# Kernel tuning notes

Measured on AMD Instinct MI355X. Metric: run time of the kernel, lower is better.

The kernel has to match this reference:

```python
import jax, jax.numpy as jnp
import numpy as np
import math

DIM = 2048
N_HEADS = 32
N_KV_HEADS = 8
HEAD_DIM = DIM // N_HEADS  # 64
N_REP = N_HEADS // N_KV_HEADS  # 4
BATCH = 1
SEQ = 2048


def rope_cos_sin(seq_len, head_dim, dtype=jnp.float32):
    inv_freq = 1.0 / (10000.0 ** (jnp.arange(0, head_dim, 2, dtype=jnp.float32) / head_dim))
    t = jnp.arange(seq_len, dtype=jnp.float32)
    freqs = jnp.outer(t, inv_freq)            # [S, D/2]
    emb = jnp.concatenate([freqs, freqs], -1)  # [S, D]
    return jnp.cos(emb).astype(dtype), jnp.sin(emb).astype(dtype)


def rotate_half(x):
    x1 = x[..., ::2]
    x2 = x[..., 1::2]
    return jnp.concatenate([-x2, x1], axis=-1)


def setup_inputs() -> dict:
    key = jax.random.key(0)
    ks = jax.random.split(key, 5)
    scale = 1.0 / math.sqrt(DIM)
    x = jax.random.normal(ks[0], (BATCH, SEQ, DIM), jnp.float32)
    wq = jax.random.normal(ks[1], (DIM, N_HEADS * HEAD_DIM), jnp.float32) * scale
    wk = jax.random.normal(ks[2], (DIM, N_KV_HEADS * HEAD_DIM), jnp.float32) * scale
    wv = jax.random.normal(ks[3], (DIM, N_KV_HEADS * HEAD_DIM), jnp.float32) * scale
    wo = jax.random.normal(ks[4], (N_HEADS * HEAD_DIM, DIM), jnp.float32) * scale
    mask = jnp.tril(jnp.ones((SEQ, SEQ), jnp.int32))[None, None]  # [1,1,S,S]
    return {"x": x, "mask": mask, "wq": wq, "wk": wk, "wv": wv, "wo": wo}


def reference(x, mask, wq, wk, wv, wo):
    B, S, _ = x.shape
    q = (x @ wq).reshape(B, S, N_HEADS, HEAD_DIM).transpose(0, 2, 1, 3)     # [B,H,S,D]
    k = (x @ wk).reshape(B, S, N_KV_HEADS, HEAD_DIM).transpose(0, 2, 1, 3)  # [B,Hkv,S,D]
    v = (x @ wv).reshape(B, S, N_KV_HEADS, HEAD_DIM).transpose(0, 2, 1, 3)
    cos, sin = rope_cos_sin(S, HEAD_DIM)  # [S,D]
    q = q * cos + rotate_half(q) * sin
    k = k * cos + rotate_half(k) * sin
    if N_REP > 1:
        k = jnp.repeat(k, N_REP, axis=1)
        v = jnp.repeat(v, N_REP, axis=1)
    scores = jnp.einsum("bhqd,bhkd->bhqk", q, k) / math.sqrt(HEAD_DIM)
    scores = jnp.where(mask == 0, -jnp.inf, scores)
    attn = jax.nn.softmax(scores, axis=-1)
    out = jnp.einsum("bhqk,bhkd->bhqd", attn, v)  # [B,H,S,D]
    out = out.transpose(0, 2, 1, 3).reshape(B, S, N_HEADS * HEAD_DIM)
    return out @ wo
```

## Files before the change

### kernel.cpp

```cpp
#include <hip/hip_runtime.h>
#include <hip/hip_bf16.h>

#define DIM 2048
#define SEQ 2048
#define NH 32
#define HD 64
#define NKV 8
#define QKV_LD 3072

typedef __attribute__((ext_vector_type(8))) short bf16x8;
typedef __attribute__((ext_vector_type(4))) float f32x4;
typedef __attribute__((ext_vector_type(2))) unsigned int uint2v;
typedef unsigned short ushort_t;

__device__ inline unsigned short f2bf(float f) {
    union { float f; unsigned int u; } v; v.f = f;
    unsigned int r = v.u + 0x7fffu + ((v.u >> 16) & 1u);
    return (unsigned short)(r >> 16);
}
__device__ inline float bf2f(ushort_t u) {
    union { unsigned int u; float f; } v; v.u = ((unsigned int)u) << 16; return v.f;
}

__device__ inline void async_cp16(const void* g, void* l) {
    __builtin_amdgcn_global_load_lds(
        (const __attribute__((address_space(1))) unsigned int*)g,
        (__attribute__((address_space(3))) unsigned int*)l, 16, 0, 0);
}

__device__ inline void pswap32(unsigned int& a, unsigned int& b) {
    uint2v r = __builtin_amdgcn_permlane32_swap(a, b, false, false);
    a = r[0]; b = r[1];
}
__device__ inline void pswap16(unsigned int& a, unsigned int& b) {
    uint2v r = __builtin_amdgcn_permlane16_swap(a, b, false, false);
    a = r[0]; b = r[1];
}
__device__ inline float wave_max(float x) {
    unsigned int a = __float_as_uint(x), b = a;
    uint2v r = __builtin_amdgcn_permlane16_swap(a, b, false, false);
    x = fmaxf(__uint_as_float(r[0]), __uint_as_float(r[1]));
    a = __float_as_uint(x); b = a;
    r = __builtin_amdgcn_permlane32_swap(a, b, false, false);
    return fmaxf(__uint_as_float(r[0]), __uint_as_float(r[1]));
}
__device__ inline float wave_sum(float x) {
    unsigned int a = __float_as_uint(x), b = a;
    uint2v r = __builtin_amdgcn_permlane16_swap(a, b, false, false);
    x = __uint_as_float(r[0]) + __uint_as_float(r[1]);
    a = __float_as_uint(x); b = a;
    r = __builtin_amdgcn_permlane32_swap(a, b, false, false);
    return __uint_as_float(r[0]) + __uint_as_float(r[1]);
}
__device__ inline unsigned int cvt_pk_bf16(float lo, float hi) {
    unsigned int r;
    asm volatile("v_cvt_pk_bf16_f32 %0, %1, %2" : "=v"(r) : "v"(lo), "v"(hi));
    return r;
}

__global__ __launch_bounds__(256) void convert_kernel(
    const float* __restrict__ X, ushort_t* __restrict__ Xb)
{
    int i = (blockIdx.x * 256 + threadIdx.x) * 4;
    float4 v = *(const float4*)(X + i);
    ushort_t o[4] = { f2bf(v.x), f2bf(v.y), f2bf(v.z), f2bf(v.w) };
    *(uint2*)(Xb + i) = *(uint2*)o;
}

__global__ __launch_bounds__(256) void transpose_kernel(
    const float* __restrict__ W, ushort_t* __restrict__ WT, int N)
{
    __shared__ __align__(16) ushort_t tile[64][72];
    const int n0 = blockIdx.x * 64, k0 = blockIdx.y * 64;
    const int t = threadIdx.x;
    {
        const int tk = t >> 4;
        const int tn = (t & 15) * 4;
        #pragma unroll
        for (int i = 0; i < 4; i++) {
            const int k = tk + i * 16;
            float4 v = *(const float4*)(W + (size_t)(k0 + k) * N + n0 + tn);
            tile[tn + 0][k] = f2bf(v.x);
            tile[tn + 1][k] = f2bf(v.y);
            tile[tn + 2][k] = f2bf(v.z);
            tile[tn + 3][k] = f2bf(v.w);
        }
    }
    __syncthreads();
    {
        const int tn = t >> 2;
        const int tk = (t & 3) * 16;
        uint4 a = *(const uint4*)&tile[tn][tk];
        uint4 b = *(const uint4*)&tile[tn][tk + 8];
        ushort_t* dst = WT + (size_t)(n0 + tn) * DIM + k0 + tk;
        *(uint4*)dst = a;
        *(uint4*)(dst + 8) = b;
    }
}

template<int OUT_F32>
__global__ __launch_bounds__(256) void gemm_kernel(
    const ushort_t* __restrict__ A, const ushort_t* __restrict__ BT,
    void* __restrict__ Cout, int K, int lda, int ldo)
{
    __shared__ __align__(16) ushort_t sA[128 * 32];
    __shared__ __align__(16) ushort_t sB[64 * 32];
    const int tn = blockIdx.x * 64, tm = blockIdx.y * 128;
    const int t = threadIdx.x, wave = t >> 6, lane = t & 63;
    const int m16 = lane & 15, quad = lane >> 4;
    const int wr = (wave >> 1) * 64, wc = (wave & 1) * 32;
    const int srow = lane >> 2;
    const int sce = (lane & 3) * 8;

    f32x4 acc[4][2] = {};

    for (int k0 = 0; k0 < K; k0 += 32) {
        __syncthreads();
        #pragma unroll
        for (int p = 0; p < 2; p++) {
            const int j = wave * 2 + p;
            const int row = j * 16 + srow;
            async_cp16(A + (size_t)(tm + row) * lda + k0 + sce, &sA[j * 512]);
        }
        async_cp16(BT + (size_t)(tn + wave * 16 + srow) * K + k0 + sce, &sB[wave * 512]);
        __syncthreads();
        bf16x8 af[4], bf[2];
        #pragma unroll
        for (int mt = 0; mt < 4; mt++)
            af[mt] = *(const bf16x8*)&sA[(wr + mt * 16 + m16) * 32 + quad * 8];
        #pragma unroll
        for (int nt = 0; nt < 2; nt++)
            bf[nt] = *(const bf16x8*)&sB[(wc + nt * 16 + m16) * 32 + quad * 8];
        #pragma unroll
        for (int mt = 0; mt < 4; mt++)
            #pragma unroll
            for (int nt = 0; nt < 2; nt++)
                acc[mt][nt] = __builtin_amdgcn_mfma_f32_16x16x32_bf16(af[mt], bf[nt], acc[mt][nt], 0, 0, 0);
    }

    #pragma unroll
    for (int mt = 0; mt < 4; mt++) {
        const int row = tm + wr + mt * 16 + quad * 4;
        #pragma unroll
        for (int nt = 0; nt < 2; nt++) {
            const int col = tn + wc + nt * 16 + m16;
            #pragma unroll
            for (int r = 0; r < 4; r++) {
                if (OUT_F32)
                    ((float*)Cout)[(size_t)(row + r) * ldo + col] = acc[mt][nt][r];
                else
                    ((ushort_t*)Cout)[(size_t)(row + r) * ldo + col] = f2bf(acc[mt][nt][r]);
            }
        }
    }
}

#define QSCALE 0.18033688011112042f
__global__ __launch_bounds__(256) void rope_kernel(ushort_t* qkv, ushort_t* __restrict__ Kr)
{
    const int gid = blockIdx.x * 256 + threadIdx.x;
    const int lane = gid & 63;
    const int idx = gid >> 6;
    const int s = idx / 40;
    const int hh = idx - s * 40;

    const ushort_t* src;
    ushort_t* dst;
    const bool isq = (hh < 32);
    if (isq) {
        dst = qkv + (size_t)s * QKV_LD + hh * 64;
        src = dst;
    } else {
        src = qkv + (size_t)s * QKV_LD + 2048 + (hh - 32) * 64;
        dst = Kr + ((size_t)(hh - 32) * SEQ + s) * 64;
    }

    const float e = bf2f(src[lane]);
    const int i = lane & 31;
    const float freq = __expf(-(float)i * 0.28782313662425572f);
    const float ang = (float)s * freq;
    const float cv = cosf(ang), sv = sinf(ang);
    const int partner = (lane < 32) ? (2 * lane + 1) : (2 * (lane - 32));
    const float y = __shfl(e, partner, 64);
    float out = (lane < 32) ? (e * cv - y * sv) : (e * cv + y * sv);
    if (isq) out *= QSCALE;
    dst[lane] = f2bf(out);
}

__global__ __launch_bounds__(256) void vtrans_kernel(
    const ushort_t* __restrict__ qkv, ushort_t* __restrict__ Vt)
{
    __shared__ __align__(16) ushort_t tile[64][72];
    const int kvh = blockIdx.x & 7;
    const int s0 = (blockIdx.x >> 3) * 64;
    const int t = threadIdx.x;
    {
        const int sr = t >> 3;
        const int d8 = (t & 7) * 8;
        #pragma unroll
        for (int i = 0; i < 2; i++) {
            const int s = sr + i * 32;
            ushort_t tmp[8];
            *(uint4*)tmp = *(const uint4*)(qkv + (size_t)(s0 + s) * QKV_LD + 2560 + kvh * 64 + d8);
            #pragma unroll
            for (int j = 0; j < 8; j++) tile[d8 + j][s] = tmp[j];
        }
    }
    __syncthreads();
    {
        const int dr = t >> 3;
        const int s8 = (t & 7) * 8;
        #pragma unroll
        for (int i = 0; i < 2; i++) {
            const int d = dr + i * 32;
            *(uint4*)(Vt + ((size_t)kvh * 64 + d) * SEQ + s0 + s8) = *(const uint4*)&tile[d][s8];
        }
    }
}

#define MFMA16(A, B, C) __builtin_amdgcn_mfma_f32_16x16x32_bf16(A, B, C, 0, 0, 0)

#define LOADK(KF, KB) do { \
    _Pragma("unroll") \
    for (int _k = 0; _k < 4; _k++) { \
        const ushort_t* _kp = Krh + (size_t)((KB) + _k * 16 + m16) * 64 + quad * 8; \
        KF[_k][0] = *(const bf16x8*)_kp; \
        KF[_k][1] = *(const bf16x8*)(_kp + 32); \
    } \
} while (0)

#define LOADV(VF, KB) do { \
    _Pragma("unroll") \
    for (int _n = 0; _n < 4; _n++) { \
        const ushort_t* _vp = Vth + (size_t)(_n * 16 + m16) * SEQ + (KB) + quad * 8; \
        VF[_n][0] = *(const bf16x8*)_vp; \
        VF[_n][1] = *(const bf16x8*)(_vp + 32); \
    } \
} while (0)

#define QKT(SC, KF, QA) do { \
    _Pragma("unroll") \
    for (int _k = 0; _k < 4; _k++) { \
        SC[_k] = MFMA16(KF[_k][0], qf[QA][0], SC[_k]); \
        SC[_k] = MFMA16(KF[_k][1], qf[QA][1], SC[_k]); \
    } \
} while (0)

#define SMPV(SC, QA, DOMASK, KBASE, VF) do { \
    float s_[16]; \
    _Pragma("unroll") \
    for (int _k = 0; _k < 4; _k++) { \
        _Pragma("unroll") \
        for (int _r = 0; _r < 4; _r++) { \
            float _v = SC[_k][_r]; \
            if ((DOMASK) && ((KBASE) + _k * 16 + quad * 4 + _r > qi[QA])) _v = -1e30f; \
            s_[_k * 4 + _r] = _v; \
        } \
    } \
    float _x0 = fmaxf(s_[0], s_[1]),   _x1 = fmaxf(s_[2], s_[3]); \
    float _x2 = fmaxf(s_[4], s_[5]),   _x3 = fmaxf(s_[6], s_[7]); \
    float _x4 = fmaxf(s_[8], s_[9]),   _x5 = fmaxf(s_[10], s_[11]); \
    float _x6 = fmaxf(s_[12], s_[13]), _x7 = fmaxf(s_[14], s_[15]); \
    float _rmax = fmaxf(fmaxf(fmaxf(_x0, _x1), fmaxf(_x2, _x3)), \
                        fmaxf(fmaxf(_x4, _x5), fmaxf(_x6, _x7))); \
    _rmax = wave_max(_rmax); \
    if (_rmax > m_run[QA] + 8.f) { \
        const float _mnew = fmaxf(m_run[QA], _rmax); \
        const float _alpha = __builtin_amdgcn_exp2f(m_run[QA] - _mnew); \
        m_run[QA] = _mnew; \
        l_run[QA] *= _alpha; \
        _Pragma("unroll") \
        for (int _n = 0; _n < 4; _n++) { \
            _Pragma("unroll") \
            for (int _r = 0; _r < 4; _r++) oacc[QA][_n][_r] *= _alpha; \
        } \
    } \
    const float _m = m_run[QA]; \
    _Pragma("unroll") \
    for (int _i = 0; _i < 16; _i++) s_[_i] = __builtin_amdgcn_exp2f(s_[_i] - _m); \
    float _y0 = s_[0] + s_[1],   _y1 = s_[2] + s_[3]; \
    float _y2 = s_[4] + s_[5],   _y3 = s_[6] + s_[7]; \
    float _y4 = s_[8] + s_[9],   _y5 = s_[10] + s_[11]; \
    float _y6 = s_[12] + s_[13], _y7 = s_[14] + s_[15]; \
    float _ps = ((_y0 + _y1) + (_y2 + _y3)) + ((_y4 + _y5) + (_y6 + _y7)); \
    l_run[QA] += wave_sum(_ps); \
    unsigned int _u00 = cvt_pk_bf16(s_[0],  s_[1]),  _u01 = cvt_pk_bf16(s_[2],  s_[3]); \
    unsigned int _u10 = cvt_pk_bf16(s_[4],  s_[5]),  _u11 = cvt_pk_bf16(s_[6],  s_[7]); \
    unsigned int _u20 = cvt_pk_bf16(s_[8],  s_[9]),  _u21 = cvt_pk_bf16(s_[10], s_[11]); \
    unsigned int _u30 = cvt_pk_bf16(s_[12], s_[13]), _u31 = cvt_pk_bf16(s_[14], s_[15]); \
    pswap32(_u00, _u10); pswap16(_u00, _u10); \
    pswap32(_u01, _u11); pswap16(_u01, _u11); \
    pswap32(_u20, _u30); pswap16(_u20, _u30); \
    pswap32(_u21, _u31); pswap16(_u21, _u31); \
    union { unsigned int w[4]; bf16x8 v; } _P0, _P1; \
    _P0.w[0] = _u00; _P0.w[1] = _u01; _P0.w[2] = _u10; _P0.w[3] = _u11; \
    _P1.w[0] = _u20; _P1.w[1] = _u21; _P1.w[2] = _u30; _P1.w[3] = _u31; \
    __builtin_amdgcn_s_setprio(1); \
    _Pragma("unroll") \
    for (int _n = 0; _n < 4; _n++) { \
        oacc[QA][_n] = MFMA16(VF[_n][0], _P0.v, oacc[QA][_n]); \
        oacc[QA][_n] = MFMA16(VF[_n][1], _P1.v, oacc[QA][_n]); \
    } \
    __builtin_amdgcn_s_setprio(0); \
} while (0)

__global__ __launch_bounds__(512, 2) void attn_kernel(
    ushort_t* qkv, const ushort_t* __restrict__ Kr, const ushort_t* __restrict__ Vt)
{
    const int t = threadIdx.x, wave = t >> 6, lane = t & 63;
    const int m16 = lane & 15, quad = lane >> 4;
    const int b = blockIdx.x;
    const int kvh = b & 7;
    const int h = kvh * 4 + ((b >> 3) & 3);
    const int p = b >> 5;
    const int grp = wave >> 2;
    const int w4 = wave & 3;
    const int band = grp ? p : 15 - p;

    const ushort_t* Krh = Kr + (size_t)kvh * SEQ * 64;
    const ushort_t* Vth = Vt + (size_t)kvh * 64 * SEQ;

    const int nkt = band * 2 + 2;

    int qi[2];
    bf16x8 qf[2][2];
    #pragma unroll
    for (int qa = 0; qa < 2; qa++) {
        qi[qa] = band * 128 + (w4 + qa * 4) * 16 + m16;
        const ushort_t* qp = qkv + (size_t)qi[qa] * QKV_LD + h * 64 + quad * 8;
        qf[qa][0] = *(const bf16x8*)qp;
        qf[qa][1] = *(const bf16x8*)(qp + 32);
    }

    f32x4 oacc[2][4] = {};
    float m_run[2] = { -1e30f, -1e30f };
    float l_run[2] = { 0.f, 0.f };

    bf16x8 kfA[4][2], kfB[4][2], vf[4][2];
    LOADK(kfA, 0);

    for (int kt = 0; kt < nkt; kt += 2) {
        const bool lastpair = (kt == nkt - 2);
        const int kb0 = kt * 64, kb1 = kb0 + 64;

        f32x4 scA0[4] = {}, scA1[4] = {};
        __builtin_amdgcn_s_setprio(1);
        QKT(scA0, kfA, 0);
        QKT(scA1, kfA, 1);
        __builtin_amdgcn_s_setprio(0);
        LOADV(vf, kb0);
        LOADK(kfB, kb1);
        SMPV(scA0, 0, lastpair, kb0, vf);
        SMPV(scA1, 1, false,    kb0, vf);

        if (!lastpair) {
            f32x4 scB0[4] = {}, scB1[4] = {};
            __builtin_amdgcn_s_setprio(1);
            QKT(scB0, kfB, 0);
            QKT(scB1, kfB, 1);
            __builtin_amdgcn_s_setprio(0);
            LOADV(vf, kb1);
            LOADK(kfA, kb1 + 64);
            SMPV(scB0, 0, false, kb1, vf);
            SMPV(scB1, 1, false, kb1, vf);
        } else {
            f32x4 scB1[4] = {};
            __builtin_amdgcn_s_setprio(1);
            QKT(scB1, kfB, 1);
            __builtin_amdgcn_s_setprio(0);
            LOADV(vf, kb1);
            SMPV(scB1, 1, true, kb1, vf);
        }
    }

    #pragma unroll
    for (int qa = 0; qa < 2; qa++) {
        const float rl = 1.f / l_run[qa];
        #pragma unroll
        for (int nt = 0; nt < 4; nt++) {
            ushort_t pk[4];
            #pragma unroll
            for (int r = 0; r < 4; r++) pk[r] = f2bf(oacc[qa][nt][r] * rl);
            *(uint2*)&qkv[(size_t)qi[qa] * QKV_LD + h * 64 + nt * 16 + quad * 4] = *(uint2*)pk;
        }
    }
}

extern "C" void kernel_launch(void* const* d_in, const int* in_sizes, int n_in,
                              void* d_out, int out_size, void* d_ws, size_t ws_size,
                              hipStream_t stream)
{
    const float* x  = (const float*)d_in[0];
    const float* wq = (const float*)d_in[2];
    const float* wk = (const float*)d_in[3];
    const float* wv = (const float*)d_in[4];
    const float* wo = (const float*)d_in[5];

    ushort_t* WT  = (ushort_t*)d_ws;
    ushort_t* xb  = WT + (size_t)3072 * 2048;
    ushort_t* woT = xb;
    ushort_t* qkv = xb + (size_t)2048 * 2048;
    ushort_t* Kr  = qkv + (size_t)SEQ * QKV_LD;
    ushort_t* Vt  = Kr + (size_t)NKV * SEQ * HD;

    dim3 blk(256);

    convert_kernel<<<(DIM * SEQ) / 1024, blk, 0, stream>>>(x, xb);
    transpose_kernel<<<dim3(32, 32), blk, 0, stream>>>(wq, WT, 2048);
    transpose_kernel<<<dim3(8, 32),  blk, 0, stream>>>(wk, WT + (size_t)2048 * 2048, 512);
    transpose_kernel<<<dim3(8, 32),  blk, 0, stream>>>(wv, WT + (size_t)2560 * 2048, 512);

    gemm_kernel<0><<<dim3(QKV_LD / 64, SEQ / 128), blk, 0, stream>>>(xb, WT, qkv, DIM, DIM, QKV_LD);

    transpose_kernel<<<dim3(32, 32), blk, 0, stream>>>(wo, woT, 2048);

    rope_kernel<<<(SEQ * 40 * 64) / 256, blk, 0, stream>>>(qkv, Kr);
    vtrans_kernel<<<NKV * (SEQ / 64), blk, 0, stream>>>(qkv, Vt);

    attn_kernel<<<8 * NH, dim3(512), 0, stream>>>(qkv, Kr, Vt);

    gemm_kernel<1><<<dim3(DIM / 64, SEQ / 128), blk, 0, stream>>>(qkv, woT, d_out, DIM, QKV_LD, DIM);
}
```

Baseline: 294.8 us.

## Double-buffer GEMM LDS tiles with K=64 swizzled stages; use hardware sin/cos in RoPE

```diff
diff --git a/kernel.cpp b/kernel.cpp
--- a/kernel.cpp
+++ b/kernel.cpp
@@ -103,53 +103,73 @@
     const ushort_t* __restrict__ A, const ushort_t* __restrict__ BT,
     void* __restrict__ Cout, int K, int lda, int ldo)
 {
-    __shared__ __align__(16) ushort_t sA[128 * 32];
-    __shared__ __align__(16) ushort_t sB[64 * 32];
+    __shared__ __align__(16) ushort_t sA[2][128 * 64];
+    __shared__ __align__(16) ushort_t sB[2][64 * 64];
     const int tn = blockIdx.x * 64, tm = blockIdx.y * 128;
     const int t = threadIdx.x, wave = t >> 6, lane = t & 63;
     const int m16 = lane & 15, quad = lane >> 4;
     const int wr = (wave >> 1) * 64, wc = (wave & 1) * 32;
-    const int srow = lane >> 2;
-    const int sce = (lane & 3) * 8;
+    const int srow = lane >> 3;
+    const int scol = ((lane & 7) ^ srow) * 8;
 
     f32x4 acc[4][2] = {};
-
-    for (int k0 = 0; k0 < K; k0 += 32) {
+    const int nsteps = K >> 6;
+
+#define GSTAGE(BUF, KO) do { \
+    _Pragma("unroll") \
+    for (int _p = 0; _p < 4; _p++) { \
+        const int _j = wave * 4 + _p; \
+        async_cp16(A + (size_t)(tm + _j * 8 + srow) * lda + (KO) + scol, &sA[BUF][_j * 512]); \
+    } \
+    _Pragma("unroll") \
+    for (int _p = 0; _p < 2; _p++) { \
+        const int _j = wave * 2 + _p; \
+        async_cp16(BT + (size_t)(tn + _j * 8 + srow) * K + (KO) + scol, &sB[BUF][_j * 512]); \
+    } \
+} while (0)
+
+    GSTAGE(0, 0);
+    int cur = 0;
+    for (int kt = 0; kt < nsteps; kt++) {
         __syncthreads();
-        #pragma unroll
-        for (int p = 0; p < 2; p++) {
-            const int j = wave * 2 + p;
-            const int row = j * 16 + srow;
-            async_cp16(A + (size_t)(tm + row) * lda + k0 + sce, &sA[j * 512]);
-        }
-        async_cp16(BT + (size_t)(tn + wave * 16 + srow) * K + k0 + sce, &sB[wave * 512]);
-        __syncthreads();
-        bf16x8 af[4], bf[2];
-        #pragma unroll
-        for (int mt = 0; mt < 4; mt++)
-            af[mt] = *(const bf16x8*)&sA[(wr + mt * 16 + m16) * 32 + quad * 8];
-        #pragma unroll
-        for (int nt = 0; nt < 2; nt++)
-            bf[nt] = *(const bf16x8*)&sB[(wc + nt * 16 + m16) * 32 + quad * 8];
-        #pragma unroll
-        for (int mt = 0; mt < 4; mt++)
-            #pragma unroll
-            for (int nt = 0; nt < 2; nt++)
-                acc[mt][nt] = __builtin_amdgcn_mfma_f32_16x16x32_bf16(af[mt], bf[nt], acc[mt][nt], 0, 0, 0);
+        if (kt + 1 < nsteps) GSTAGE(cur ^ 1, (kt + 1) * 64);
+        bf16x8 af[4][2], bf[2][2];
+        #pragma unroll
+        for (int mt = 0; mt < 4; mt++) {
+            const int row = wr + mt * 16 + m16;
+            #pragma unroll
+            for (int kk = 0; kk < 2; kk++)
+                af[mt][kk] = *(const bf16x8*)&sA[cur][row * 64 + ((kk * 4 + quad) ^ (m16 & 7)) * 8];
+        }
+        #pragma unroll
+        for (int nt2 = 0; nt2 < 2; nt2++) {
+            const int row = wc + nt2 * 16 + m16;
+            #pragma unroll
+            for (int kk = 0; kk < 2; kk++)
+                bf[nt2][kk] = *(const bf16x8*)&sB[cur][row * 64 + ((kk * 4 + quad) ^ (m16 & 7)) * 8];
+        }
+        #pragma unroll
+        for (int kk = 0; kk < 2; kk++)
+            #pragma unroll
+            for (int mt = 0; mt < 4; mt++)
+                #pragma unroll
+                for (int nt2 = 0; nt2 < 2; nt2++)
+                    acc[mt][nt2] = __builtin_amdgcn_mfma_f32_16x16x32_bf16(af[mt][kk], bf[nt2][kk], acc[mt][nt2], 0, 0, 0);
+        cur ^= 1;
     }
 
     #pragma unroll
     for (int mt = 0; mt < 4; mt++) {
         const int row = tm + wr + mt * 16 + quad * 4;
         #pragma unroll
-        for (int nt = 0; nt < 2; nt++) {
-            const int col = tn + wc + nt * 16 + m16;
+        for (int nt2 = 0; nt2 < 2; nt2++) {
+            const int col = tn + wc + nt2 * 16 + m16;
             #pragma unroll
             for (int r = 0; r < 4; r++) {
                 if (OUT_F32)
-                    ((float*)Cout)[(size_t)(row + r) * ldo + col] = acc[mt][nt][r];
+                    ((float*)Cout)[(size_t)(row + r) * ldo + col] = acc[mt][nt2][r];
                 else
-                    ((ushort_t*)Cout)[(size_t)(row + r) * ldo + col] = f2bf(acc[mt][nt][r]);
+                    ((ushort_t*)Cout)[(size_t)(row + r) * ldo + col] = f2bf(acc[mt][nt2][r]);
             }
         }
     }
@@ -177,9 +197,12 @@
 
     const float e = bf2f(src[lane]);
     const int i = lane & 31;
-    const float freq = __expf(-(float)i * 0.28782313662425572f);
-    const float ang = (float)s * freq;
-    const float cv = cosf(ang), sv = sinf(ang);
+    const float freq_rev = __builtin_amdgcn_exp2f(-(float)i * 0.4152410118609203f)
+                           * 0.15915494309189535f;
+    float fr = (float)s * freq_rev;
+    fr = fr - floorf(fr);
+    const float cv = __builtin_amdgcn_cosf(fr);
+    const float sv = __builtin_amdgcn_sinf(fr);
     const int partner = (lane < 32) ? (2 * lane + 1) : (2 * (lane - 32));
     const float y = __shfl(e, partner, 64);
     float out = (lane < 32) ? (e * cv - y * sv) : (e * cv + y * sv);
```

Result: faster. 259.5 us (-12.0%).
